# Optimization experiments

Measured on AMD Instinct MI355X. Metric: run time of the kernel, lower is better.

## Reference

```python
import jax, jax.numpy as jnp
import numpy as np

D_MODEL = 1024
D_FF = 4096
N_HEADS = 16
D_HEAD = D_MODEL // N_HEADS
BSZ, SEQ = 2, 2048
EPS = 1e-6


def layer_norm(x, lam, beta):
    # torch impl: (x - mu) / (std_biased + eps) * lambda + beta
    mu = jnp.mean(x, axis=-1, keepdims=True)
    sigma = jnp.sqrt(jnp.mean((x - mu) ** 2, axis=-1, keepdims=True)) + EPS
    return (x - mu) / sigma * lam + beta


def setup_inputs() -> dict:
    key = jax.random.key(0)
    ks = jax.random.split(key, 10)
    s = 0.02
    x = jax.random.normal(ks[0], (BSZ, SEQ, D_MODEL), dtype=jnp.float32)
    mask = jnp.ones((BSZ, 1, 1, SEQ), dtype=jnp.int32)
    # nn.Linear weights stored [out, in]; y = x @ W.T
    Wq = jax.random.normal(ks[1], (D_MODEL, D_MODEL), dtype=jnp.float32) * s
    Wk = jax.random.normal(ks[2], (D_MODEL, D_MODEL), dtype=jnp.float32) * s
    Wv = jax.random.normal(ks[3], (D_MODEL, D_MODEL), dtype=jnp.float32) * s
    Wo = jax.random.normal(ks[4], (D_MODEL, D_MODEL), dtype=jnp.float32) * s
    w1 = jax.random.normal(ks[5], (D_FF, D_MODEL), dtype=jnp.float32) * s
    b1 = jnp.zeros((D_FF,), dtype=jnp.float32)
    w2 = jax.random.normal(ks[6], (D_MODEL, D_FF), dtype=jnp.float32) * s
    b2 = jnp.zeros((D_MODEL,), dtype=jnp.float32)
    g1 = jnp.ones((D_MODEL,), dtype=jnp.float32)
    be1 = jnp.zeros((D_MODEL,), dtype=jnp.float32)
    g2 = jnp.ones((D_MODEL,), dtype=jnp.float32)
    be2 = jnp.zeros((D_MODEL,), dtype=jnp.float32)
    return {"x": x, "mask": mask, "Wq": Wq, "Wk": Wk, "Wv": Wv, "Wo": Wo,
            "w1": w1, "b1": b1, "w2": w2, "b2": b2,
            "g1": g1, "be1": be1, "g2": g2, "be2": be2}


def reference(x, mask, Wq, Wk, Wv, Wo, w1, b1, w2, b2, g1, be1, g2, be2):
    b, s, _ = x.shape
    # projections (y = x @ W.T), split heads -> [b, h, s, dh]
    def split_heads(t):
        return t.reshape(b, s, N_HEADS, D_HEAD).transpose(0, 2, 1, 3)
    Q = split_heads(x @ Wq.T)
    K = split_heads(x @ Wk.T)
    V = split_heads(x @ Wv.T)
    score = jnp.einsum('bhqd,bhkd->bhqk', Q, K) / jnp.sqrt(jnp.float32(D_HEAD))
    score = jnp.where(mask == 0, -jnp.inf, score)
    attn = jax.nn.softmax(score, axis=-1)
    out = jnp.einsum('bhqk,bhkd->bhqd', attn, V)
    out = out.transpose(0, 2, 1, 3).reshape(b, s, D_MODEL)
    x1 = out @ Wo.T
    x2 = layer_norm(x1 + x, g1, be1)
    x3 = jax.nn.relu(x2 @ w1.T + b1) @ w2.T + b2
    x4 = layer_norm(x2 + x3, g2, be2)
    return x4
```

## Files before the change

kernel.cpp:

```cpp
#include <hip/hip_runtime.h>
#include <math.h>

typedef __attribute__((ext_vector_type(8))) short bf16x8;
typedef __attribute__((ext_vector_type(4))) float f32x4;
typedef __attribute__((ext_vector_type(8))) unsigned short us8;
typedef unsigned short u16;
typedef unsigned int u32;

constexpr int BSZ = 2, SEQ = 2048, DM = 1024, DFF = 4096, NH = 16, DH = 64;
constexpr int MROWS = BSZ * SEQ;

__device__ __forceinline__ float bf2f(u16 u) {
  union { unsigned int i; float f; } v; v.i = ((unsigned int)u) << 16; return v.f;
}
__device__ __forceinline__ u16 f2bf(float f) {
  union { float f; unsigned int i; } v; v.f = f;
  unsigned int r = v.i + 0x7fffu + ((v.i >> 16) & 1u);
  return (u16)(r >> 16);
}

#define GLOAD16(gp, lp) __builtin_amdgcn_global_load_lds( \
    (const __attribute__((address_space(1))) void*)(gp),  \
    (__attribute__((address_space(3))) void*)(lp), 16, 0, 0)
#define GLOAD4(gp, lp) __builtin_amdgcn_global_load_lds( \
    (const __attribute__((address_space(1))) void*)(gp),  \
    (__attribute__((address_space(3))) void*)(lp), 4, 0, 0)

__global__ __launch_bounds__(256) void cvt_all(
    const float* __restrict__ x, const float* __restrict__ Wq,
    const float* __restrict__ Wk, const float* __restrict__ Wv,
    const float* __restrict__ Wo, const float* __restrict__ w1,
    const float* __restrict__ w2, u16* __restrict__ xb,
    u16* __restrict__ Wqkvb, u16* __restrict__ Wob,
    u16* __restrict__ w1b, u16* __restrict__ w2b) {
  constexpr int M1 = 1 << 20;
  const int i = (blockIdx.x * 256 + threadIdx.x) * 8;
  const float* src;
  u16* dst;
  int off;
  if (i < 4 * M1)        { src = x;  dst = xb;            off = i;           }
  else if (i < 5 * M1)   { src = Wq; dst = Wqkvb;         off = i - 4 * M1;  }
  else if (i < 6 * M1)   { src = Wk; dst = Wqkvb + M1;    off = i - 5 * M1;  }
  else if (i < 7 * M1)   { src = Wv; dst = Wqkvb + 2 * M1; off = i - 6 * M1; }
  else if (i < 8 * M1)   { src = Wo; dst = Wob;           off = i - 7 * M1;  }
  else if (i < 12 * M1)  { src = w1; dst = w1b;           off = i - 8 * M1;  }
  else                   { src = w2; dst = w2b;           off = i - 12 * M1; }
  const float4 a = *(const float4*)(src + off);
  const float4 b = *(const float4*)(src + off + 4);
  uint4 o;
  o.x = f2bf(a.x) | ((unsigned)f2bf(a.y) << 16);
  o.y = f2bf(a.z) | ((unsigned)f2bf(a.w) << 16);
  o.z = f2bf(b.x) | ((unsigned)f2bf(b.y) << 16);
  o.w = f2bf(b.z) | ((unsigned)f2bf(b.w) << 16);
  *(uint4*)(dst + off) = o;
}

template <int BM, int BN, bool BIAS, bool RELU, bool OBF16>
__global__ __launch_bounds__(256) void gemm_bf16(
    const u16* __restrict__ A, const u16* __restrict__ B,
    const float* __restrict__ bias, float* __restrict__ Cf,
    u16* __restrict__ Cb, int M, int N, int K) {
  constexpr int MI = BM / 32, NI = BN / 32;
  __shared__ u16 As[2][BM * 32];
  __shared__ u16 Bs[2][BN * 32];
  const int tid = threadIdx.x;
  const int lane = tid & 63, wid = tid >> 6;

  const int nwg = gridDim.x * gridDim.y;
  int id = blockIdx.y * gridDim.x + blockIdx.x;
  id = (id & 7) * (nwg >> 3) + (id >> 3);
  const int bx = id % gridDim.x, by = id / gridDim.x;

  const int row0 = by * BM, col0 = bx * BN;
  const int wr = (wid >> 1) * (BM / 2), wc = (wid & 1) * (BN / 2);
  const int fr = lane & 15, hi = lane >> 4;

  f32x4 acc[MI][NI];
#pragma unroll
  for (int i = 0; i < MI; ++i)
#pragma unroll
    for (int j = 0; j < NI; ++j) acc[i][j] = {0.f, 0.f, 0.f, 0.f};

  const int sr = tid >> 2;
  const int se = (tid & 3) * 8;

#define STAGE(buf, k0)                                                        \
  {                                                                           \
    _Pragma("unroll")                                                         \
    for (int c = 0; c < BM * 64; c += 4096) {                                 \
      const int r = (c >> 6) + sr;                                            \
      GLOAD16(A + (size_t)(row0 + r) * K + ((k0) + se),                       \
              ((char*)As[buf]) + c + tid * 16);                               \
    }                                                                         \
    _Pragma("unroll")                                                         \
    for (int c = 0; c < BN * 64; c += 4096) {                                 \
      const int r = (c >> 6) + sr;                                            \
      GLOAD16(B + (size_t)(col0 + r) * K + ((k0) + se),                       \
              ((char*)Bs[buf]) + c + tid * 16);                               \
    }                                                                         \
  }

  STAGE(0, 0);
  __syncthreads();

  const int NIT = K / 32;
  for (int it = 0; it < NIT; ++it) {
    const int cur = it & 1;
    if (it + 1 < NIT) STAGE(cur ^ 1, (it + 1) * 32);

    bf16x8 af[MI], bv[NI];
#pragma unroll
    for (int mi = 0; mi < MI; ++mi)
      af[mi] = *(const bf16x8*)&As[cur][(wr + mi * 16 + fr) * 32 + hi * 8];
#pragma unroll
    for (int ni = 0; ni < NI; ++ni)
      bv[ni] = *(const bf16x8*)&Bs[cur][(wc + ni * 16 + fr) * 32 + hi * 8];
#pragma unroll
    for (int mi = 0; mi < MI; ++mi)
#pragma unroll
      for (int ni = 0; ni < NI; ++ni)
        acc[mi][ni] = __builtin_amdgcn_mfma_f32_16x16x32_bf16(
            af[mi], bv[ni], acc[mi][ni], 0, 0, 0);
    __syncthreads();
  }
#undef STAGE

  const int erow = row0 + wr + (hi << 2);
  const int ecol0 = col0 + wc;
#pragma unroll
  for (int ni = 0; ni < NI; ++ni) {
    const int col = ecol0 + ni * 16 + fr;
    const float bvv = BIAS ? bias[col] : 0.f;
#pragma unroll
    for (int mi = 0; mi < MI; ++mi) {
      const int rbase = erow + mi * 16;
#pragma unroll
      for (int j = 0; j < 4; ++j) {
        float v = acc[mi][ni][j] + bvv;
        if (RELU) v = fmaxf(v, 0.f);
        const size_t idx = (size_t)(rbase + j) * N + col;
        if (OBF16) Cb[idx] = f2bf(v); else Cf[idx] = v;
      }
    }
  }
}

__global__ __launch_bounds__(256) void attn_mfma(
    const u16* __restrict__ QKV, const int* __restrict__ mask,
    u16* __restrict__ Ob) {
  constexpr int KB = 64, QB = 64, NT = SEQ / KB;
  __shared__ u16 Kl[2][KB * 64];
  __shared__ u16 Vt[2][64 * KB];
  __shared__ int ml[2][KB];

  const int tid = threadIdx.x;
  const int lane = tid & 63, wid = tid >> 6;
  const int q0 = blockIdx.x * QB;
  const int bh = blockIdx.y;
  const int b = bh >> 4, h = bh & 15;
  const size_t base = (size_t)b * SEQ * 3072;
  const int fr = lane & 15, g = lane >> 4;

  const u16* qp = QKV + base + (size_t)(q0 + wid * 16 + fr) * 3072 + h * 64 + g * 8;
  const bf16x8 qf0 = *(const bf16x8*)qp;
  const bf16x8 qf1 = *(const bf16x8*)(qp + 32);

  const int krow = wid * 16 + (lane >> 3);
  const int kcol = 8 * ((lane & 7) ^ (lane >> 3));
  const u16* ksrc = QKV + base + 1024 + h * 64 + kcol;
  const int kdst = wid * 2048 + lane * 16;

  const int va = tid >> 3;
  const int vq = tid & 7;
  const u16* vsrc = QKV + base + 2048 + h * 64 + vq * 8;

  f32x4 o[4] = {{0.f,0.f,0.f,0.f},{0.f,0.f,0.f,0.f},{0.f,0.f,0.f,0.f},{0.f,0.f,0.f,0.f}};
  float mreg = -3e38f, lreg = 0.f;

  {
    GLOAD16(ksrc + (size_t)krow * 3072, (char*)Kl[0] + kdst);
    GLOAD16(ksrc + (size_t)(krow + 8) * 3072, (char*)Kl[0] + kdst + 1024);
    if (wid == 0) GLOAD4(mask + b * SEQ + lane, (char*)ml[0] + lane * 4);
    const us8 v0 = *(const us8*)(vsrc + (size_t)(2 * va) * 3072);
    const us8 v1 = *(const us8*)(vsrc + (size_t)(2 * va + 1) * 3072);
    char* vb = (char*)Vt[0];
#pragma unroll
    for (int i = 0; i < 8; ++i) {
      const int d = vq * 8 + i;
      const u32 wv = (u32)(u16)v0[i] | ((u32)(u16)v1[i] << 16);
      *(u32*)(vb + d * 128 + ((4 * va) ^ ((vq ^ i) << 4))) = wv;
    }
  }
  __syncthreads();

  for (int it = 0; it < NT; ++it) {
    const int cur = it & 1, nxt = cur ^ 1;
    const int ktn = (it + 1) * KB;
    const bool pre = (it + 1 < NT);
    us8 v0 = {}, v1 = {};
    if (pre) {
      GLOAD16(ksrc + (size_t)(ktn + krow) * 3072, (char*)Kl[nxt] + kdst);
      GLOAD16(ksrc + (size_t)(ktn + krow + 8) * 3072, (char*)Kl[nxt] + kdst + 1024);
      if (wid == 0) GLOAD4(mask + b * SEQ + ktn + lane, (char*)ml[nxt] + lane * 4);
      v0 = *(const us8*)(vsrc + (size_t)(ktn + 2 * va) * 3072);
      v1 = *(const us8*)(vsrc + (size_t)(ktn + 2 * va + 1) * 3072);
    }

    f32x4 s[4];
#pragma unroll
    for (int t16 = 0; t16 < 4; ++t16) {
      const int kr = t16 * 16 + fr;
      const char* krp = (const char*)Kl[cur] + kr * 128;
      const int sw = (kr & 7) << 4;
      const bf16x8 kf0 = *(const bf16x8*)(krp + ((g * 16) ^ sw));
      const bf16x8 kf1 = *(const bf16x8*)(krp + ((g * 16 + 64) ^ sw));
      f32x4 a = {0.f, 0.f, 0.f, 0.f};
      a = __builtin_amdgcn_mfma_f32_16x16x32_bf16(kf0, qf0, a, 0, 0, 0);
      a = __builtin_amdgcn_mfma_f32_16x16x32_bf16(kf1, qf1, a, 0, 0, 0);
      s[t16] = a;
    }

#pragma unroll
    for (int t16 = 0; t16 < 4; ++t16) {
      const int4 mv = *(const int4*)&ml[cur][t16 * 16 + g * 4];
      const int* mp = (const int*)&mv;
#pragma unroll
      for (int j = 0; j < 4; ++j)
        s[t16][j] = (mp[j] == 0) ? -3e38f : s[t16][j] * 0.125f;
    }

    float rmax = s[0][0];
#pragma unroll
    for (int t16 = 0; t16 < 4; ++t16)
#pragma unroll
      for (int j = 0; j < 4; ++j) rmax = fmaxf(rmax, s[t16][j]);
    rmax = fmaxf(rmax, __shfl_xor(rmax, 16));
    rmax = fmaxf(rmax, __shfl_xor(rmax, 32));

    if (!__all(rmax <= mreg + 8.f)) {
      const float mn = fmaxf(mreg, rmax);
      const float sc = __expf(mreg - mn);
      mreg = mn;
      lreg *= sc;
#pragma unroll
      for (int j = 0; j < 4; ++j) {
        const float scj = __shfl(sc, (g << 4) + g * 4 + j);
#pragma unroll
        for (int dt = 0; dt < 4; ++dt) o[dt][j] *= scj;
      }
    }

    float p[4][4];
    float rsum = 0.f;
#pragma unroll
    for (int t16 = 0; t16 < 4; ++t16)
#pragma unroll
      for (int j = 0; j < 4; ++j) {
        p[t16][j] = __expf(s[t16][j] - mreg);
        rsum += p[t16][j];
      }
    rsum += __shfl_xor(rsum, 16);
    rsum += __shfl_xor(rsum, 32);
    lreg += rsum;

    u32 plo[4], phi[4];
#pragma unroll
    for (int t16 = 0; t16 < 4; ++t16) {
      asm("v_cvt_pk_bf16_f32 %0, %1, %2"
          : "=v"(plo[t16]) : "v"(p[t16][0]), "v"(p[t16][1]));
      asm("v_cvt_pk_bf16_f32 %0, %1, %2"
          : "=v"(phi[t16]) : "v"(p[t16][2]), "v"(p[t16][3]));
    }

#pragma unroll
    for (int kh = 0; kh < 2; ++kh) {
      u32 fd[4];
#pragma unroll
      for (int hf = 0; hf < 2; ++hf) {
        const int sl = fr + ((((g & 1) << 1) + hf) << 4);
        const u32 c0l = (u32)__shfl((int)plo[kh * 2], sl);
        const u32 c0h = (u32)__shfl((int)phi[kh * 2], sl);
        const u32 c1l = (u32)__shfl((int)plo[kh * 2 + 1], sl);
        const u32 c1h = (u32)__shfl((int)phi[kh * 2 + 1], sl);
        const bool s1 = ((g >> 1) & 1) != 0;
        fd[hf * 2] = s1 ? c1l : c0l;
        fd[hf * 2 + 1] = s1 ? c1h : c0h;
      }
      union { u32 d[4]; bf16x8 v; } uu;
      uu.d[0] = fd[0]; uu.d[1] = fd[1]; uu.d[2] = fd[2]; uu.d[3] = fd[3];
      const bf16x8 pf = uu.v;
#pragma unroll
      for (int dt = 0; dt < 4; ++dt) {
        const int d = dt * 16 + fr;
        const int xd = (((d >> 3) ^ d) & 7) << 4;
        const bf16x8 vf = *(const bf16x8*)((const char*)Vt[cur] + d * 128 +
                                           ((g * 16 + kh * 64) ^ xd));
        o[dt] = __builtin_amdgcn_mfma_f32_16x16x32_bf16(pf, vf, o[dt], 0, 0, 0);
      }
    }

    if (pre) {
      char* vb = (char*)Vt[nxt];
#pragma unroll
      for (int i = 0; i < 8; ++i) {
        const int d = vq * 8 + i;
        const u32 wv = (u32)(u16)v0[i] | ((u32)(u16)v1[i] << 16);
        *(u32*)(vb + d * 128 + ((4 * va) ^ ((vq ^ i) << 4))) = wv;
      }
    }
    __syncthreads();
  }

  const float inv = 1.f / lreg;
#pragma unroll
  for (int j = 0; j < 4; ++j) {
    const float invj = __shfl(inv, (g << 4) + g * 4 + j);
    const int qrow = q0 + wid * 16 + g * 4 + j;
    u16* orow = Ob + (size_t)(b * SEQ + qrow) * DM + h * 64;
#pragma unroll
    for (int dt = 0; dt < 4; ++dt)
      orow[dt * 16 + fr] = f2bf(o[dt][j] * invj);
  }
}

template <bool ABF, bool BBF, bool OBF>
__global__ __launch_bounds__(256) void ln_add(const void* __restrict__ Ap,
                                              const void* __restrict__ Bp,
                                              const float* __restrict__ g,
                                              const float* __restrict__ be,
                                              void* __restrict__ outp) {
  __shared__ float red[2][4];
  __shared__ float mu_s, sig_s;
  const int row = blockIdx.x;
  const int tid = threadIdx.x;

  float4 a, b;
  if (ABF) {
    const ushort4 u = *(const ushort4*)((const u16*)Ap + (size_t)row * DM + tid * 4);
    a = make_float4(bf2f(u.x), bf2f(u.y), bf2f(u.z), bf2f(u.w));
  } else {
    a = *(const float4*)((const float*)Ap + (size_t)row * DM + tid * 4);
  }
  if (BBF) {
    const ushort4 u = *(const ushort4*)((const u16*)Bp + (size_t)row * DM + tid * 4);
    b = make_float4(bf2f(u.x), bf2f(u.y), bf2f(u.z), bf2f(u.w));
  } else {
    b = *(const float4*)((const float*)Bp + (size_t)row * DM + tid * 4);
  }
  float4 s = make_float4(a.x + b.x, a.y + b.y, a.z + b.z, a.w + b.w);

  float sum = s.x + s.y + s.z + s.w;
  float sq = s.x * s.x + s.y * s.y + s.z * s.z + s.w * s.w;
#pragma unroll
  for (int off = 32; off >= 1; off >>= 1) {
    sum += __shfl_xor(sum, off);
    sq += __shfl_xor(sq, off);
  }
  const int wid = tid >> 6;
  if ((tid & 63) == 0) { red[0][wid] = sum; red[1][wid] = sq; }
  __syncthreads();
  if (tid == 0) {
    float ts = red[0][0] + red[0][1] + red[0][2] + red[0][3];
    float tq = red[1][0] + red[1][1] + red[1][2] + red[1][3];
    float mu = ts * (1.f / DM);
    float var = tq * (1.f / DM) - mu * mu;
    mu_s = mu;
    sig_s = sqrtf(fmaxf(var, 0.f)) + 1e-6f;
  }
  __syncthreads();
  const float mu = mu_s, inv = 1.f / sig_s;
  const float4 gv = *(const float4*)(g + tid * 4);
  const float4 bv = *(const float4*)(be + tid * 4);
  float4 o;
  o.x = (s.x - mu) * inv * gv.x + bv.x;
  o.y = (s.y - mu) * inv * gv.y + bv.y;
  o.z = (s.z - mu) * inv * gv.z + bv.z;
  o.w = (s.w - mu) * inv * gv.w + bv.w;
  if (OBF) {
    u16* op = (u16*)outp + (size_t)row * DM + tid * 4;
    ushort4 o4;
    o4.x = f2bf(o.x); o4.y = f2bf(o.y); o4.z = f2bf(o.z); o4.w = f2bf(o.w);
    *(ushort4*)op = o4;
  } else {
    *(float4*)((float*)outp + (size_t)row * DM + tid * 4) = o;
  }
}

extern "C" void kernel_launch(void* const* d_in, const int* in_sizes, int n_in,
                              void* d_out, int out_size, void* d_ws,
                              size_t ws_size, hipStream_t stream) {
  const float* x  = (const float*)d_in[0];
  const int* mask = (const int*)d_in[1];
  const float* Wq = (const float*)d_in[2];
  const float* Wk = (const float*)d_in[3];
  const float* Wv = (const float*)d_in[4];
  const float* Wo = (const float*)d_in[5];
  const float* w1 = (const float*)d_in[6];
  const float* b1 = (const float*)d_in[7];
  const float* w2 = (const float*)d_in[8];
  const float* b2 = (const float*)d_in[9];
  const float* g1 = (const float*)d_in[10];
  const float* be1 = (const float*)d_in[11];
  const float* g2 = (const float*)d_in[12];
  const float* be2 = (const float*)d_in[13];
  float* out = (float*)d_out;
  float* ws = (float*)d_ws;

  u16*   QKVb  = (u16*)(ws + 0);
  u16*   xb    = (u16*)(ws + 6291456);
  u16*   Wqkvb = (u16*)(ws + 8388608);
  u16*   Wob   = (u16*)(ws + 9961472);
  u16*   w1b   = (u16*)(ws + 10485760);
  u16*   w2b   = (u16*)(ws + 12582912);
  u16*   Obf   = (u16*)(ws + 14680064);
  u16*   X1b   = (u16*)(ws + 16777216);
  u16*   X2b   = (u16*)(ws + 20971520);
  u16*   X3b   = (u16*)(ws + 23068672);
  u16*   Hb    = (u16*)(ws + 0);

  const dim3 blk(256);

  cvt_all<<<8192, blk, 0, stream>>>(x, Wq, Wk, Wv, Wo, w1, w2,
                                    xb, Wqkvb, Wob, w1b, w2b);

  gemm_bf16<128, 128, false, false, true><<<dim3(3072 / 128, MROWS / 128), blk, 0, stream>>>(
      xb, Wqkvb, nullptr, nullptr, QKVb, MROWS, 3072, DM);

  attn_mfma<<<dim3(SEQ / 64, BSZ * NH), blk, 0, stream>>>(QKVb, mask, Obf);

  gemm_bf16<64, 128, false, false, true><<<dim3(DM / 128, MROWS / 64), blk, 0, stream>>>(
      Obf, Wob, nullptr, nullptr, X1b, MROWS, DM, DM);

  ln_add<true, false, true><<<dim3(MROWS), blk, 0, stream>>>(X1b, x, g1, be1, X2b);

  gemm_bf16<128, 128, true, true, true><<<dim3(DFF / 128, MROWS / 128), blk, 0, stream>>>(
      X2b, w1b, b1, nullptr, Hb, MROWS, DFF, DM);

  gemm_bf16<64, 128, true, false, true><<<dim3(DM / 128, MROWS / 64), blk, 0, stream>>>(
      Hb, w2b, b2, nullptr, X3b, MROWS, DM, DFF);

  ln_add<true, true, false><<<dim3(MROWS), blk, 0, stream>>>(X2b, X3b, g2, be2, out);
}
```

Baseline: 304.6 us.

## Enlarge attention query block to 128 with 8 waves and trim softmax work

The attention kernel now runs 512 threads per block covering 128 query rows, so each K/V tile staged in shared memory is reused by twice as many waves. Q is pre-scaled by log2(e)/sqrt(dh) so the softmax can use raw v_exp_f32 (base-2) without a per-score multiply. The row-max cross-lane shuffles move inside the rare rescale branch (threshold raised to 12), and the row-sum reduction is deferred to the end of the loop. In exchange, Q is rounded to bf16 after scaling, the lazy-rescale bound is looser, and there are half as many blocks to schedule.

```diff
diff --git a/kernel.cpp b/kernel.cpp
--- a/kernel.cpp
+++ b/kernel.cpp
@@ -145,10 +145,10 @@
   }
 }
 
-__global__ __launch_bounds__(256) void attn_mfma(
+__global__ __launch_bounds__(512) void attn_mfma(
     const u16* __restrict__ QKV, const int* __restrict__ mask,
     u16* __restrict__ Ob) {
-  constexpr int KB = 64, QB = 64, NT = SEQ / KB;
+  constexpr int KB = 64, QB = 128, NT = SEQ / KB;
   __shared__ u16 Kl[2][KB * 64];
   __shared__ u16 Vt[2][64 * KB];
   __shared__ int ml[2][KB];
@@ -162,33 +162,51 @@
   const int fr = lane & 15, g = lane >> 4;
 
   const u16* qp = QKV + base + (size_t)(q0 + wid * 16 + fr) * 3072 + h * 64 + g * 8;
-  const bf16x8 qf0 = *(const bf16x8*)qp;
-  const bf16x8 qf1 = *(const bf16x8*)(qp + 32);
-
-  const int krow = wid * 16 + (lane >> 3);
+  bf16x8 qf0, qf1;
+  {
+    const float QSC = 0.18033688f;
+    const us8 ua = *(const us8*)qp;
+    const us8 ub = *(const us8*)(qp + 32);
+    u32 pa[4], pb[4];
+#pragma unroll
+    for (int i = 0; i < 4; ++i) {
+      const float a0 = bf2f(ua[2 * i]) * QSC, a1 = bf2f(ua[2 * i + 1]) * QSC;
+      const float b0 = bf2f(ub[2 * i]) * QSC, b1 = bf2f(ub[2 * i + 1]) * QSC;
+      asm("v_cvt_pk_bf16_f32 %0, %1, %2" : "=v"(pa[i]) : "v"(a0), "v"(a1));
+      asm("v_cvt_pk_bf16_f32 %0, %1, %2" : "=v"(pb[i]) : "v"(b0), "v"(b1));
+    }
+    union { u32 d[4]; bf16x8 v; } c0, c1;
+#pragma unroll
+    for (int i = 0; i < 4; ++i) { c0.d[i] = pa[i]; c1.d[i] = pb[i]; }
+    qf0 = c0.v; qf1 = c1.v;
+  }
+
+  const int krow = wid * 8 + (lane >> 3);
   const int kcol = 8 * ((lane & 7) ^ (lane >> 3));
   const u16* ksrc = QKV + base + 1024 + h * 64 + kcol;
-  const int kdst = wid * 2048 + lane * 16;
-
-  const int va = tid >> 3;
+  const int kdst = wid * 1024 + lane * 16;
+
+  const int va = (tid & 255) >> 3;
   const int vq = tid & 7;
   const u16* vsrc = QKV + base + 2048 + h * 64 + vq * 8;
+  const bool vstage = (wid < 4);
 
   f32x4 o[4] = {{0.f,0.f,0.f,0.f},{0.f,0.f,0.f,0.f},{0.f,0.f,0.f,0.f},{0.f,0.f,0.f,0.f}};
   float mreg = -3e38f, lreg = 0.f;
 
   {
     GLOAD16(ksrc + (size_t)krow * 3072, (char*)Kl[0] + kdst);
-    GLOAD16(ksrc + (size_t)(krow + 8) * 3072, (char*)Kl[0] + kdst + 1024);
-    if (wid == 0) GLOAD4(mask + b * SEQ + lane, (char*)ml[0] + lane * 4);
-    const us8 v0 = *(const us8*)(vsrc + (size_t)(2 * va) * 3072);
-    const us8 v1 = *(const us8*)(vsrc + (size_t)(2 * va + 1) * 3072);
-    char* vb = (char*)Vt[0];
-#pragma unroll
-    for (int i = 0; i < 8; ++i) {
-      const int d = vq * 8 + i;
-      const u32 wv = (u32)(u16)v0[i] | ((u32)(u16)v1[i] << 16);
-      *(u32*)(vb + d * 128 + ((4 * va) ^ ((vq ^ i) << 4))) = wv;
+    if (wid == 4) GLOAD4(mask + b * SEQ + lane, (char*)ml[0] + lane * 4);
+    if (vstage) {
+      const us8 v0 = *(const us8*)(vsrc + (size_t)(2 * va) * 3072);
+      const us8 v1 = *(const us8*)(vsrc + (size_t)(2 * va + 1) * 3072);
+      char* vb = (char*)Vt[0];
+#pragma unroll
+      for (int i = 0; i < 8; ++i) {
+        const int d = vq * 8 + i;
+        const u32 wv = (u32)(u16)v0[i] | ((u32)(u16)v1[i] << 16);
+        *(u32*)(vb + d * 128 + ((4 * va) ^ ((vq ^ i) << 4))) = wv;
+      }
     }
   }
   __syncthreads();
@@ -200,10 +218,11 @@
     us8 v0 = {}, v1 = {};
     if (pre) {
       GLOAD16(ksrc + (size_t)(ktn + krow) * 3072, (char*)Kl[nxt] + kdst);
-      GLOAD16(ksrc + (size_t)(ktn + krow + 8) * 3072, (char*)Kl[nxt] + kdst + 1024);
-      if (wid == 0) GLOAD4(mask + b * SEQ + ktn + lane, (char*)ml[nxt] + lane * 4);
-      v0 = *(const us8*)(vsrc + (size_t)(ktn + 2 * va) * 3072);
-      v1 = *(const us8*)(vsrc + (size_t)(ktn + 2 * va + 1) * 3072);
+      if (wid == 4) GLOAD4(mask + b * SEQ + ktn + lane, (char*)ml[nxt] + lane * 4);
+      if (vstage) {
+        v0 = *(const us8*)(vsrc + (size_t)(ktn + 2 * va) * 3072);
+        v1 = *(const us8*)(vsrc + (size_t)(ktn + 2 * va + 1) * 3072);
+      }
     }
 
     f32x4 s[4];
@@ -226,7 +245,7 @@
       const int* mp = (const int*)&mv;
 #pragma unroll
       for (int j = 0; j < 4; ++j)
-        s[t16][j] = (mp[j] == 0) ? -3e38f : s[t16][j] * 0.125f;
+        if (mp[j] == 0) s[t16][j] = -3e38f;
     }
 
     float rmax = s[0][0];
@@ -234,12 +253,13 @@
     for (int t16 = 0; t16 < 4; ++t16)
 #pragma unroll
       for (int j = 0; j < 4; ++j) rmax = fmaxf(rmax, s[t16][j]);
-    rmax = fmaxf(rmax, __shfl_xor(rmax, 16));
-    rmax = fmaxf(rmax, __shfl_xor(rmax, 32));
-
-    if (!__all(rmax <= mreg + 8.f)) {
+
+    if (!__all(rmax <= mreg + 12.f)) {
+      rmax = fmaxf(rmax, __shfl_xor(rmax, 16));
+      rmax = fmaxf(rmax, __shfl_xor(rmax, 32));
       const float mn = fmaxf(mreg, rmax);
-      const float sc = __expf(mreg - mn);
+      float sc;
+      asm("v_exp_f32 %0, %1" : "=v"(sc) : "v"(mreg - mn));
       mreg = mn;
       lreg *= sc;
 #pragma unroll
@@ -251,17 +271,15 @@
     }
 
     float p[4][4];
-    float rsum = 0.f;
 #pragma unroll
     for (int t16 = 0; t16 < 4; ++t16)
 #pragma unroll
       for (int j = 0; j < 4; ++j) {
-        p[t16][j] = __expf(s[t16][j] - mreg);
-        rsum += p[t16][j];
-      }
-    rsum += __shfl_xor(rsum, 16);
-    rsum += __shfl_xor(rsum, 32);
-    lreg += rsum;
+        float e;
+        asm("v_exp_f32 %0, %1" : "=v"(e) : "v"(s[t16][j] - mreg));
+        p[t16][j] = e;
+        lreg += e;
+      }
 
     u32 plo[4], phi[4];
 #pragma unroll
@@ -299,7 +317,7 @@
       }
     }
 
-    if (pre) {
+    if (pre && vstage) {
       char* vb = (char*)Vt[nxt];
 #pragma unroll
       for (int i = 0; i < 8; ++i) {
@@ -311,6 +329,8 @@
     __syncthreads();
   }
 
+  lreg += __shfl_xor(lreg, 16);
+  lreg += __shfl_xor(lreg, 32);
   const float inv = 1.f / lreg;
 #pragma unroll
   for (int j = 0; j < 4; ++j) {
@@ -426,7 +446,7 @@
   gemm_bf16<128, 128, false, false, true><<<dim3(3072 / 128, MROWS / 128), blk, 0, stream>>>(
       xb, Wqkvb, nullptr, nullptr, QKVb, MROWS, 3072, DM);
 
-  attn_mfma<<<dim3(SEQ / 64, BSZ * NH), blk, 0, stream>>>(QKVb, mask, Obf);
+  attn_mfma<<<dim3(SEQ / 128, BSZ * NH), dim3(512), 0, stream>>>(QKVb, mask, Obf);
 
   gemm_bf16<64, 128, false, false, true><<<dim3(DM / 128, MROWS / 64), blk, 0, stream>>>(
       Obf, Wob, nullptr, nullptr, X1b, MROWS, DM, DM);
```

Result: faster. 271.6 us (-10.8%).

## Process two 16-row query tiles per wave in attention to reuse K/V loads

Applied to the files above, without the earlier changes.

Each attention wave now handles 32 query rows (two independent 16-row tiles with separate softmax state), doubling the query block to 128 and halving the grid, so every K/V tile in LDS and every K/V fragment read is reused across twice as many MFMAs. The softmax scale and log2(e) are folded into Q at load time so the raw v_exp_f32 (exp2) can be used, the per-iteration row-sum shuffle is deferred to the end, and the rescale threshold is relaxed. This raises register pressure (launch bounds set to 4 blocks per CU) and halves the number of blocks, which may hurt occupancy and load balance.

```diff
diff --git a/kernel.cpp b/kernel.cpp
--- a/kernel.cpp
+++ b/kernel.cpp
@@ -145,10 +145,10 @@
   }
 }
 
-__global__ __launch_bounds__(256) void attn_mfma(
+__global__ __launch_bounds__(256, 4) void attn_mfma(
     const u16* __restrict__ QKV, const int* __restrict__ mask,
     u16* __restrict__ Ob) {
-  constexpr int KB = 64, QB = 64, NT = SEQ / KB;
+  constexpr int KB = 64, QB = 128, NT = SEQ / KB;
   __shared__ u16 Kl[2][KB * 64];
   __shared__ u16 Vt[2][64 * KB];
   __shared__ int ml[2][KB];
@@ -161,21 +161,36 @@
   const size_t base = (size_t)b * SEQ * 3072;
   const int fr = lane & 15, g = lane >> 4;
 
-  const u16* qp = QKV + base + (size_t)(q0 + wid * 16 + fr) * 3072 + h * 64 + g * 8;
-  const bf16x8 qf0 = *(const bf16x8*)qp;
-  const bf16x8 qf1 = *(const bf16x8*)(qp + 32);
+  const float QSC = 0.18033688f;
+  auto loadq = [&](const u16* p) -> bf16x8 {
+    const us8 u = *(const us8*)p;
+    u32 d[4];
+#pragma unroll
+    for (int i = 0; i < 4; ++i) {
+      const float a0 = bf2f(u[2 * i]) * QSC, a1 = bf2f(u[2 * i + 1]) * QSC;
+      asm("v_cvt_pk_bf16_f32 %0, %1, %2" : "=v"(d[i]) : "v"(a0), "v"(a1));
+    }
+    union { u32 d[4]; bf16x8 v; } c;
+#pragma unroll
+    for (int i = 0; i < 4; ++i) c.d[i] = d[i];
+    return c.v;
+  };
+  const u16* qpA = QKV + base + (size_t)(q0 + wid * 32 + fr) * 3072 + h * 64 + g * 8;
+  const u16* qpB = qpA + (size_t)16 * 3072;
+  const bf16x8 qfA0 = loadq(qpA), qfA1 = loadq(qpA + 32);
+  const bf16x8 qfB0 = loadq(qpB), qfB1 = loadq(qpB + 32);
 
   const int krow = wid * 16 + (lane >> 3);
   const int kcol = 8 * ((lane & 7) ^ (lane >> 3));
   const u16* ksrc = QKV + base + 1024 + h * 64 + kcol;
   const int kdst = wid * 2048 + lane * 16;
 
-  const int va = tid >> 3;
-  const int vq = tid & 7;
+  const int va = tid >> 3, vq = tid & 7;
   const u16* vsrc = QKV + base + 2048 + h * 64 + vq * 8;
 
-  f32x4 o[4] = {{0.f,0.f,0.f,0.f},{0.f,0.f,0.f,0.f},{0.f,0.f,0.f,0.f},{0.f,0.f,0.f,0.f}};
-  float mreg = -3e38f, lreg = 0.f;
+  f32x4 oA[4] = {{0,0,0,0},{0,0,0,0},{0,0,0,0},{0,0,0,0}};
+  f32x4 oB[4] = {{0,0,0,0},{0,0,0,0},{0,0,0,0},{0,0,0,0}};
+  float mA = -3e38f, lA = 0.f, mB = -3e38f, lB = 0.f;
 
   {
     GLOAD16(ksrc + (size_t)krow * 3072, (char*)Kl[0] + kdst);
@@ -206,7 +221,7 @@
       v1 = *(const us8*)(vsrc + (size_t)(ktn + 2 * va + 1) * 3072);
     }
 
-    f32x4 s[4];
+    f32x4 sA[4], sB[4];
 #pragma unroll
     for (int t16 = 0; t16 < 4; ++t16) {
       const int kr = t16 * 16 + fr;
@@ -215,9 +230,13 @@
       const bf16x8 kf0 = *(const bf16x8*)(krp + ((g * 16) ^ sw));
       const bf16x8 kf1 = *(const bf16x8*)(krp + ((g * 16 + 64) ^ sw));
       f32x4 a = {0.f, 0.f, 0.f, 0.f};
-      a = __builtin_amdgcn_mfma_f32_16x16x32_bf16(kf0, qf0, a, 0, 0, 0);
-      a = __builtin_amdgcn_mfma_f32_16x16x32_bf16(kf1, qf1, a, 0, 0, 0);
-      s[t16] = a;
+      a = __builtin_amdgcn_mfma_f32_16x16x32_bf16(kf0, qfA0, a, 0, 0, 0);
+      a = __builtin_amdgcn_mfma_f32_16x16x32_bf16(kf1, qfA1, a, 0, 0, 0);
+      sA[t16] = a;
+      f32x4 c = {0.f, 0.f, 0.f, 0.f};
+      c = __builtin_amdgcn_mfma_f32_16x16x32_bf16(kf0, qfB0, c, 0, 0, 0);
+      c = __builtin_amdgcn_mfma_f32_16x16x32_bf16(kf1, qfB1, c, 0, 0, 0);
+      sB[t16] = c;
     }
 
 #pragma unroll
@@ -226,76 +245,109 @@
       const int* mp = (const int*)&mv;
 #pragma unroll
       for (int j = 0; j < 4; ++j)
-        s[t16][j] = (mp[j] == 0) ? -3e38f : s[t16][j] * 0.125f;
-    }
-
-    float rmax = s[0][0];
-#pragma unroll
-    for (int t16 = 0; t16 < 4; ++t16)
-#pragma unroll
-      for (int j = 0; j < 4; ++j) rmax = fmaxf(rmax, s[t16][j]);
-    rmax = fmaxf(rmax, __shfl_xor(rmax, 16));
-    rmax = fmaxf(rmax, __shfl_xor(rmax, 32));
-
-    if (!__all(rmax <= mreg + 8.f)) {
-      const float mn = fmaxf(mreg, rmax);
-      const float sc = __expf(mreg - mn);
-      mreg = mn;
-      lreg *= sc;
-#pragma unroll
-      for (int j = 0; j < 4; ++j) {
-        const float scj = __shfl(sc, (g << 4) + g * 4 + j);
-#pragma unroll
-        for (int dt = 0; dt < 4; ++dt) o[dt][j] *= scj;
-      }
-    }
-
-    float p[4][4];
-    float rsum = 0.f;
-#pragma unroll
-    for (int t16 = 0; t16 < 4; ++t16)
-#pragma unroll
-      for (int j = 0; j < 4; ++j) {
-        p[t16][j] = __expf(s[t16][j] - mreg);
-        rsum += p[t16][j];
-      }
-    rsum += __shfl_xor(rsum, 16);
-    rsum += __shfl_xor(rsum, 32);
-    lreg += rsum;
-
-    u32 plo[4], phi[4];
-#pragma unroll
-    for (int t16 = 0; t16 < 4; ++t16) {
-      asm("v_cvt_pk_bf16_f32 %0, %1, %2"
-          : "=v"(plo[t16]) : "v"(p[t16][0]), "v"(p[t16][1]));
-      asm("v_cvt_pk_bf16_f32 %0, %1, %2"
-          : "=v"(phi[t16]) : "v"(p[t16][2]), "v"(p[t16][3]));
+        if (mp[j] == 0) { sA[t16][j] = -3e38f; sB[t16][j] = -3e38f; }
+    }
+
+    u32 ploA[4], phiA[4], ploB[4], phiB[4];
+    {
+      float rmax = sA[0][0];
+#pragma unroll
+      for (int t16 = 0; t16 < 4; ++t16)
+#pragma unroll
+        for (int j = 0; j < 4; ++j) rmax = fmaxf(rmax, sA[t16][j]);
+      if (!__all(rmax <= mA + 12.f)) {
+        rmax = fmaxf(rmax, __shfl_xor(rmax, 16));
+        rmax = fmaxf(rmax, __shfl_xor(rmax, 32));
+        const float mn = fmaxf(mA, rmax);
+        float sc;
+        asm("v_exp_f32 %0, %1" : "=v"(sc) : "v"(mA - mn));
+        mA = mn;
+        lA *= sc;
+#pragma unroll
+        for (int j = 0; j < 4; ++j) {
+          const float scj = __shfl(sc, (g << 4) + g * 4 + j);
+#pragma unroll
+          for (int dt = 0; dt < 4; ++dt) oA[dt][j] *= scj;
+        }
+      }
+#pragma unroll
+      for (int t16 = 0; t16 < 4; ++t16) {
+        float p0, p1, p2, p3;
+        asm("v_exp_f32 %0, %1" : "=v"(p0) : "v"(sA[t16][0] - mA));
+        asm("v_exp_f32 %0, %1" : "=v"(p1) : "v"(sA[t16][1] - mA));
+        asm("v_exp_f32 %0, %1" : "=v"(p2) : "v"(sA[t16][2] - mA));
+        asm("v_exp_f32 %0, %1" : "=v"(p3) : "v"(sA[t16][3] - mA));
+        lA += (p0 + p1) + (p2 + p3);
+        asm("v_cvt_pk_bf16_f32 %0, %1, %2" : "=v"(ploA[t16]) : "v"(p0), "v"(p1));
+        asm("v_cvt_pk_bf16_f32 %0, %1, %2" : "=v"(phiA[t16]) : "v"(p2), "v"(p3));
+      }
+    }
+    {
+      float rmax = sB[0][0];
+#pragma unroll
+      for (int t16 = 0; t16 < 4; ++t16)
+#pragma unroll
+        for (int j = 0; j < 4; ++j) rmax = fmaxf(rmax, sB[t16][j]);
+      if (!__all(rmax <= mB + 12.f)) {
+        rmax = fmaxf(rmax, __shfl_xor(rmax, 16));
+        rmax = fmaxf(rmax, __shfl_xor(rmax, 32));
+        const float mn = fmaxf(mB, rmax);
+        float sc;
+        asm("v_exp_f32 %0, %1" : "=v"(sc) : "v"(mB - mn));
+        mB = mn;
+        lB *= sc;
+#pragma unroll
+        for (int j = 0; j < 4; ++j) {
+          const float scj = __shfl(sc, (g << 4) + g * 4 + j);
+#pragma unroll
+          for (int dt = 0; dt < 4; ++dt) oB[dt][j] *= scj;
+        }
+      }
+#pragma unroll
+      for (int t16 = 0; t16 < 4; ++t16) {
+        float p0, p1, p2, p3;
+        asm("v_exp_f32 %0, %1" : "=v"(p0) : "v"(sB[t16][0] - mB));
+        asm("v_exp_f32 %0, %1" : "=v"(p1) : "v"(sB[t16][1] - mB));
+        asm("v_exp_f32 %0, %1" : "=v"(p2) : "v"(sB[t16][2] - mB));
+        asm("v_exp_f32 %0, %1" : "=v"(p3) : "v"(sB[t16][3] - mB));
+        lB += (p0 + p1) + (p2 + p3);
+        asm("v_cvt_pk_bf16_f32 %0, %1, %2" : "=v"(ploB[t16]) : "v"(p0), "v"(p1));
+        asm("v_cvt_pk_bf16_f32 %0, %1, %2" : "=v"(phiB[t16]) : "v"(p2), "v"(p3));
+      }
     }
 
 #pragma unroll
     for (int kh = 0; kh < 2; ++kh) {
-      u32 fd[4];
+      const bool s1 = ((g >> 1) & 1) != 0;
+      u32 fdA[4], fdB[4];
 #pragma unroll
       for (int hf = 0; hf < 2; ++hf) {
         const int sl = fr + ((((g & 1) << 1) + hf) << 4);
-        const u32 c0l = (u32)__shfl((int)plo[kh * 2], sl);
-        const u32 c0h = (u32)__shfl((int)phi[kh * 2], sl);
-        const u32 c1l = (u32)__shfl((int)plo[kh * 2 + 1], sl);
-        const u32 c1h = (u32)__shfl((int)phi[kh * 2 + 1], sl);
-        const bool s1 = ((g >> 1) & 1) != 0;
-        fd[hf * 2] = s1 ? c1l : c0l;
-        fd[hf * 2 + 1] = s1 ? c1h : c0h;
-      }
-      union { u32 d[4]; bf16x8 v; } uu;
-      uu.d[0] = fd[0]; uu.d[1] = fd[1]; uu.d[2] = fd[2]; uu.d[3] = fd[3];
-      const bf16x8 pf = uu.v;
+        const u32 a0l = (u32)__shfl((int)ploA[kh * 2], sl);
+        const u32 a0h = (u32)__shfl((int)phiA[kh * 2], sl);
+        const u32 a1l = (u32)__shfl((int)ploA[kh * 2 + 1], sl);
+        const u32 a1h = (u32)__shfl((int)phiA[kh * 2 + 1], sl);
+        fdA[hf * 2] = s1 ? a1l : a0l;
+        fdA[hf * 2 + 1] = s1 ? a1h : a0h;
+        const u32 b0l = (u32)__shfl((int)ploB[kh * 2], sl);
+        const u32 b0h = (u32)__shfl((int)phiB[kh * 2], sl);
+        const u32 b1l = (u32)__shfl((int)ploB[kh * 2 + 1], sl);
+        const u32 b1h = (u32)__shfl((int)phiB[kh * 2 + 1], sl);
+        fdB[hf * 2] = s1 ? b1l : b0l;
+        fdB[hf * 2 + 1] = s1 ? b1h : b0h;
+      }
+      union { u32 d[4]; bf16x8 v; } ua, ub;
+#pragma unroll
+      for (int i = 0; i < 4; ++i) { ua.d[i] = fdA[i]; ub.d[i] = fdB[i]; }
+      const bf16x8 pfA = ua.v, pfB = ub.v;
 #pragma unroll
       for (int dt = 0; dt < 4; ++dt) {
         const int d = dt * 16 + fr;
         const int xd = (((d >> 3) ^ d) & 7) << 4;
         const bf16x8 vf = *(const bf16x8*)((const char*)Vt[cur] + d * 128 +
                                            ((g * 16 + kh * 64) ^ xd));
-        o[dt] = __builtin_amdgcn_mfma_f32_16x16x32_bf16(pf, vf, o[dt], 0, 0, 0);
+        oA[dt] = __builtin_amdgcn_mfma_f32_16x16x32_bf16(pfA, vf, oA[dt], 0, 0, 0);
+        oB[dt] = __builtin_amdgcn_mfma_f32_16x16x32_bf16(pfB, vf, oB[dt], 0, 0, 0);
       }
     }
 
@@ -311,15 +363,24 @@
     __syncthreads();
   }
 
-  const float inv = 1.f / lreg;
+  lA += __shfl_xor(lA, 16);
+  lA += __shfl_xor(lA, 32);
+  lB += __shfl_xor(lB, 16);
+  lB += __shfl_xor(lB, 32);
+  const float invA = 1.f / lA, invB = 1.f / lB;
 #pragma unroll
   for (int j = 0; j < 4; ++j) {
-    const float invj = __shfl(inv, (g << 4) + g * 4 + j);
-    const int qrow = q0 + wid * 16 + g * 4 + j;
-    u16* orow = Ob + (size_t)(b * SEQ + qrow) * DM + h * 64;
-#pragma unroll
-    for (int dt = 0; dt < 4; ++dt)
-      orow[dt * 16 + fr] = f2bf(o[dt][j] * invj);
+    const int sl = (g << 4) + g * 4 + j;
+    const float iA = __shfl(invA, sl);
+    const float iB = __shfl(invB, sl);
+    const int qrA = q0 + wid * 32 + g * 4 + j;
+    u16* orA = Ob + (size_t)(b * SEQ + qrA) * DM + h * 64;
+    u16* orB = orA + (size_t)16 * DM;
+#pragma unroll
+    for (int dt = 0; dt < 4; ++dt) {
+      orA[dt * 16 + fr] = f2bf(oA[dt][j] * iA);
+      orB[dt * 16 + fr] = f2bf(oB[dt][j] * iB);
+    }
   }
 }
 
@@ -426,7 +487,7 @@
   gemm_bf16<128, 128, false, false, true><<<dim3(3072 / 128, MROWS / 128), blk, 0, stream>>>(
       xb, Wqkvb, nullptr, nullptr, QKVb, MROWS, 3072, DM);
 
-  attn_mfma<<<dim3(SEQ / 64, BSZ * NH), blk, 0, stream>>>(QKVb, mask, Obf);
+  attn_mfma<<<dim3(SEQ / 128, BSZ * NH), blk, 0, stream>>>(QKVb, mask, Obf);
 
   gemm_bf16<64, 128, false, false, true><<<dim3(DM / 128, MROWS / 64), blk, 0, stream>>>(
       Obf, Wob, nullptr, nullptr, X1b, MROWS, DM, DM);
```

Measured after the change: 340.8 us. 11.9% more time.
